# Performance work log

Measured on AMD Instinct MI355X. Metric: run time of the kernel, lower is better.

The kernel has to match this reference:

```python
import jax, jax.numpy as jnp
import numpy as np

CDIM = 32
SCALES = (1, 16, 64, 256, 1024, 4096)  # last entry == T
INV_TEMP = 100.0
ENT_W = 0.1
COMMIT_W = 0.2
Q_SCALE = 1.0 / float(np.sqrt(CDIM))


def _interp_area(x, pt):
    # x: [B, T, C] -> [B, pt, C]; T divisible by pt so 'area' == block mean
    B, T, C = x.shape
    return x.reshape(B, pt, T // pt, C).mean(axis=2)


def _interp_linear(x, T):
    # x: [B, pt, C] -> [B, T, C]; mode='linear', align_corners=False
    pt = x.shape[1]
    pos = (jnp.arange(T, dtype=jnp.float32) + 0.5) * (pt / T) - 0.5
    pos = jnp.clip(pos, 0.0, pt - 1.0)
    lo = jnp.floor(pos).astype(jnp.int32)
    hi = jnp.minimum(lo + 1, pt - 1)
    w = (pos - lo.astype(jnp.float32))[None, :, None]
    return x[:, lo] * (1.0 - w) + x[:, hi] * w


def _bsq(f):
    # L2 normalize (torch F.normalize: clamp_min on norm)
    f = f / jnp.maximum(jnp.linalg.norm(f, axis=-1, keepdims=True), 1e-12)
    # sign quantize with STE
    zhat = jnp.where(f > 0, Q_SCALE, -Q_SCALE).astype(f.dtype)
    quantized = f + jax.lax.stop_gradient(zhat - f)
    # soft entropy loss
    p = jax.nn.sigmoid(-4.0 * f * (INV_TEMP / float(np.sqrt(CDIM))))
    prob = jnp.stack([p, 1.0 - p], axis=-1)  # [B, T, C, 2]
    ent = lambda c: -(c * jnp.log(c + 1e-8)).sum(axis=-1)
    per_sample_entropy = ent(prob).sum(axis=-1).mean()
    avg_prob = prob.mean(axis=(0, 1))  # [C, 2]
    cb_entropy = ent(avg_prob).sum()
    entropy_penalty = (per_sample_entropy - cb_entropy) / INV_TEMP
    commit = ((jax.lax.stop_gradient(quantized) - f) ** 2).sum(axis=-1).mean()
    aux = entropy_penalty * ENT_W + commit * COMMIT_W
    bits = (quantized > 0).astype(jnp.int32)
    return quantized, bits, aux


def setup_inputs() -> dict:
    key = jax.random.key(0)
    B, T, C = 128, SCALES[-1], CDIM
    return {"f_BTC": jax.random.normal(key, (B, T, C), dtype=jnp.float32)}


def reference(f_BTC):
    B, T, C = f_BTC.shape
    quantized_out = jnp.zeros_like(f_BTC)
    residual = f_BTC
    losses, bit_list = [], []
    for pt in SCALES:
        interp_res = _interp_area(residual, pt) if pt != T else residual
        q, bits, loss = _bsq(interp_res)
        q = _interp_linear(q, T) if pt != T else q
        residual = residual - jax.lax.stop_gradient(q)
        quantized_out = quantized_out + q
        bit_list.append(bits)
        losses.append(loss)
    all_losses = jnp.stack(losses, axis=-1)       # [num_scales]
    all_bits = jnp.concatenate(bit_list, axis=1)  # [B, sum(SCALES), C]
    return quantized_out, all_bits, all_losses
```

## Files before the change

### kernel.cpp

```cpp
#include <hip/hip_runtime.h>
#include <hip/hip_bf16.h>
#include <cstddef>
#include <cstdint>

#define NB 128
#define NT 4096
#define NC 32
#define BITROWS 5457
#define QV_ROWS 1361
#define QOUT_ELEMS (NB*NT*NC)
#define BITS_ELEMS (NB*BITROWS*NC)

#define ACC_OFF  22298624
#define S16_OFF  22302720

__device__ __constant__ float kQSC = 0.17677669529663687f;
__device__ __constant__ float kSIG = 17.67766952966369f;

__device__ __forceinline__ float interp_eval(const float* __restrict__ q, int P, int t, int c) {
  float pos = ((float)t + 0.5f) * ((float)P * (1.0f / 4096.0f)) - 0.5f;
  pos = fminf(fmaxf(pos, 0.0f), (float)(P - 1));
  const int lo = (int)pos;
  const int hi = min(lo + 1, P - 1);
  const float w = pos - (float)lo;
  const float a = __fmul_rn(q[lo * NC + c], 1.0f - w);
  const float b = __fmul_rn(q[hi * NC + c], w);
  return __fadd_rn(a, b);
}

__device__ __forceinline__ void process_elem(
    float msum, float invn, int b, int rowOff, int j, int c,
    float* qlsRow, float* __restrict__ qvG, float* __restrict__ bitsG,
    float& entA, float& comA, float& pA)
{
  const float m = msum * invn;
  float ss = m * m;
  #pragma unroll
  for (int mk = 16; mk; mk >>= 1) ss += __shfl_xor(ss, mk, 32);
  const float den = fmaxf(sqrtf(ss), 1e-12f);
  const float fn = m / den;
  const bool bit = fn > 0.0f;
  const float zh = bit ? kQSC : -kQSC;
  const float qvv = fn + (zh - fn);
  if (qlsRow) qlsRow[c] = qvv;
  qvG[(size_t)b * (QV_ROWS * NC) + (size_t)(rowOff + j) * NC + c] = qvv;
  bitsG[(size_t)b * (BITROWS * NC) + (size_t)(rowOff + j) * NC + c] = bit ? 1.0f : 0.0f;
  const float arg = (-4.0f * fn) * kSIG;
  const float p = 1.0f / (1.0f + __expf(-arg));
  const float ent = -(p * __logf(p + 1e-8f) + (1.0f - p) * __logf((1.0f - p) + 1e-8f));
  const float d = qvv - fn;
  entA += ent; comA += d * d; pA += p;
}

__device__ __forceinline__ void reduce_losses(
    int sIdx, float entA, float comA, float pA, int tid, int nWaves,
    double* __restrict__ acc, float* redE, float* redC, float* redP)
{
  float e = entA, cm = comA;
  #pragma unroll
  for (int mk = 32; mk; mk >>= 1) { e += __shfl_xor(e, mk, 64); cm += __shfl_xor(cm, mk, 64); }
  const float p = pA + __shfl_xor(pA, 32, 64);
  const int w = tid >> 6, lane = tid & 63;
  if (lane == 0) { redE[w] = e; redC[w] = cm; }
  if (lane < 32) redP[w * 32 + lane] = p;
  __syncthreads();
  if (tid == 0) {
    double te = 0.0, tc = 0.0;
    for (int i = 0; i < nWaves; ++i) { te += (double)redE[i]; tc += (double)redC[i]; }
    atomicAdd(&acc[sIdx], te);
    atomicAdd(&acc[6 + sIdx], tc);
  }
  if (tid < 32) {
    float tp = 0.0f;
    for (int i = 0; i < nWaves; ++i) tp += redP[i * 32 + tid];
    atomicAdd(&acc[12 + sIdx * 32 + tid], (double)tp);
  }
  __syncthreads();
}

__global__ __launch_bounds__(256) void k_sum16(const float* __restrict__ f, float* __restrict__ S16) {
  const int idx = blockIdx.x * 256 + threadIdx.x;
  if (idx >= NB * 256 * NC) return;
  const int c = idx & 31;
  const int j = (idx >> 5) & 255;
  const int b = idx >> 13;
  const float* p = f + (size_t)b * (NT * NC) + (size_t)j * 16 * NC + c;
  float s = 0.0f;
  #pragma unroll
  for (int k = 0; k < 16; ++k) s += p[k * NC];
  S16[idx] = s;
}

__global__ __launch_bounds__(1024) void k_coarse(
    const float* __restrict__ S16g, float* __restrict__ qv,
    float* __restrict__ bitsOut, double* __restrict__ acc)
{
  __shared__ float S[256 * NC];
  __shared__ float qls[81 * NC];
  __shared__ float red[1024];
  __shared__ float redE[16], redC[16], redP[16 * 32];
  const int b = blockIdx.x, tid = threadIdx.x;
  const int c = tid & 31;

  for (int e = tid; e < 256 * NC; e += 1024) S[e] = S16g[(size_t)b * 8192 + e];
  __syncthreads();

  float entA, comA, pA;

  entA = comA = pA = 0.0f;
  {
    const int g = tid >> 5;
    float part = 0.0f;
    #pragma unroll
    for (int j = 0; j < 8; ++j) part += S[(g * 8 + j) * NC + c];
    red[tid] = part;
  }
  __syncthreads();
  if (tid < 32) {
    float msum = 0.0f;
    for (int g = 0; g < 32; ++g) msum += red[g * 32 + tid];
    process_elem(msum, 1.0f / 4096.0f, b, 0, 0, tid, &qls[0], qv, bitsOut, entA, comA, pA);
  }
  reduce_losses(0, entA, comA, pA, tid, 16, acc, redE, redC, redP);
  {
    const float corr = 16.0f * qls[c];
    for (int e = tid; e < 8192; e += 1024) S[e] -= corr;
  }
  __syncthreads();

  entA = comA = pA = 0.0f;
  if (tid < 512) {
    const int j = tid >> 5;
    float msum = 0.0f;
    for (int jj = 0; jj < 16; ++jj) msum += S[(j * 16 + jj) * NC + c];
    process_elem(msum, 1.0f / 256.0f, b, 1, j, c, &qls[(1 + j) * NC], qv, bitsOut, entA, comA, pA);
  }
  reduce_losses(1, entA, comA, pA, tid, 16, acc, redE, redC, redP);
  for (int e = tid; e < 8192; e += 1024) {
    const int jj = e >> 5;
    float cs = 0.0f;
    #pragma unroll
    for (int k = 0; k < 16; ++k) cs += interp_eval(&qls[1 * NC], 16, jj * 16 + k, c);
    S[e] -= cs;
  }
  __syncthreads();

  entA = comA = pA = 0.0f;
  for (int out = tid; out < 2048; out += 1024) {
    const int j = out >> 5;
    float msum = 0.0f;
    #pragma unroll
    for (int jj = 0; jj < 4; ++jj) msum += S[(j * 4 + jj) * NC + c];
    process_elem(msum, 1.0f / 64.0f, b, 17, j, c, &qls[(17 + j) * NC], qv, bitsOut, entA, comA, pA);
  }
  reduce_losses(2, entA, comA, pA, tid, 16, acc, redE, redC, redP);
  for (int e = tid; e < 8192; e += 1024) {
    const int jj = e >> 5;
    float cs = 0.0f;
    #pragma unroll
    for (int k = 0; k < 16; ++k) cs += interp_eval(&qls[17 * NC], 64, jj * 16 + k, c);
    S[e] -= cs;
  }
  __syncthreads();

  entA = comA = pA = 0.0f;
  for (int out = tid; out < 8192; out += 1024) {
    const int j = out >> 5;
    process_elem(S[out], 1.0f / 16.0f, b, 81, j, c, nullptr, qv, bitsOut, entA, comA, pA);
  }
  reduce_losses(3, entA, comA, pA, tid, 16, acc, redE, redC, redP);
}

__global__ __launch_bounds__(256) void k_scale4(
    const float* __restrict__ f, float* __restrict__ qv,
    float* __restrict__ bitsOut, double* __restrict__ acc)
{
  __shared__ float ql[337 * NC];
  __shared__ float redE[16], redC[16], redP[16 * 32];
  const int b = blockIdx.x >> 4, seg = blockIdx.x & 15;
  const int tid = threadIdx.x, c = tid & 31, rloc = tid >> 5;
  for (int e = tid; e < 337 * NC; e += 256) ql[e] = qv[(size_t)b * (QV_ROWS * NC) + e];
  __syncthreads();
  float entA = 0.0f, comA = 0.0f, pA = 0.0f;
  for (int pass = 0; pass < 8; ++pass) {
    const int i = seg * 64 + pass * 8 + rloc;
    const float* fp = f + (size_t)b * (NT * NC) + (size_t)i * 4 * NC + c;
    float msum = 0.0f;
    #pragma unroll
    for (int k = 0; k < 4; ++k) {
      const int t = i * 4 + k;
      float r = fp[k * NC];
      r -= interp_eval(&ql[0],        1,   t, c);
      r -= interp_eval(&ql[1 * NC],   16,  t, c);
      r -= interp_eval(&ql[17 * NC],  64,  t, c);
      r -= interp_eval(&ql[81 * NC],  256, t, c);
      msum += r;
    }
    process_elem(msum, 0.25f, b, 337, i, c, nullptr, qv, bitsOut, entA, comA, pA);
  }
  reduce_losses(4, entA, comA, pA, tid, 4, acc, redE, redC, redP);
}

__global__ __launch_bounds__(256) void k_final(
    const float* __restrict__ f, const float* __restrict__ qv,
    float* __restrict__ qout, float* __restrict__ bitsOut, double* __restrict__ acc)
{
  __shared__ float ql[337 * NC];
  __shared__ float ql4[66 * NC];
  __shared__ float redE[16], redC[16], redP[16 * 32];
  const int b = blockIdx.x >> 4, seg = blockIdx.x & 15;
  const int tid = threadIdx.x, c = tid & 31, rloc = tid >> 5;
  const int t0 = seg * 256;
  for (int e = tid; e < 337 * NC; e += 256) ql[e] = qv[(size_t)b * (QV_ROWS * NC) + e];
  const int lo0 = max(0, t0 / 4 - 1);
  const int lo1 = min(1023, t0 / 4 + 64);
  const int n4 = (lo1 - lo0 + 1) * NC;
  for (int e = tid; e < n4; e += 256)
    ql4[e] = qv[(size_t)b * (QV_ROWS * NC) + (size_t)(337 + lo0) * NC + e];
  __syncthreads();
  float entA = 0.0f, comA = 0.0f, pA = 0.0f;
  for (int pass = 0; pass < 32; ++pass) {
    const int t = t0 + pass * 8 + rloc;
    const float fv = f[(size_t)b * (NT * NC) + (size_t)t * NC + c];
    const float q0 = interp_eval(&ql[0],       1,   t, c);
    const float q1 = interp_eval(&ql[1 * NC],  16,  t, c);
    const float q2 = interp_eval(&ql[17 * NC], 64,  t, c);
    const float q3 = interp_eval(&ql[81 * NC], 256, t, c);
    float pos = ((float)t + 0.5f) * 0.25f - 0.5f;
    pos = fminf(fmaxf(pos, 0.0f), 1023.0f);
    const int lo = (int)pos;
    const int hi = min(lo + 1, 1023);
    const float w = pos - (float)lo;
    const float q4 = __fadd_rn(__fmul_rn(ql4[(lo - lo0) * NC + c], 1.0f - w),
                               __fmul_rn(ql4[(hi - lo0) * NC + c], w));
    float r = fv;
    r -= q0; r -= q1; r -= q2; r -= q3; r -= q4;
    float qs = q0; qs += q1; qs += q2; qs += q3; qs += q4;
    float ss = r * r;
    #pragma unroll
    for (int mk = 16; mk; mk >>= 1) ss += __shfl_xor(ss, mk, 32);
    const float den = fmaxf(sqrtf(ss), 1e-12f);
    const float fn = r / den;
    const bool bit = fn > 0.0f;
    const float zh = bit ? kQSC : -kQSC;
    const float qvv = fn + (zh - fn);
    qout[(size_t)b * (NT * NC) + (size_t)t * NC + c] = qs + qvv;
    bitsOut[(size_t)b * (BITROWS * NC) + (size_t)(1361 + t) * NC + c] = bit ? 1.0f : 0.0f;
    const float arg = (-4.0f * fn) * kSIG;
    const float p = 1.0f / (1.0f + __expf(-arg));
    entA += -(p * __logf(p + 1e-8f) + (1.0f - p) * __logf((1.0f - p) + 1e-8f));
    const float d = qvv - fn;
    comA += d * d;
    pA += p;
  }
  reduce_losses(5, entA, comA, pA, tid, 4, acc, redE, redC, redP);
}

__global__ void k_losses(const double* __restrict__ acc, float* __restrict__ out) {
  const int s = threadIdx.x;
  if (s >= 6) return;
  const int pts[6] = {1, 16, 64, 256, 1024, 4096};
  const double n = 128.0 * (double)pts[s];
  const double pse = acc[s] / n;
  const double commit = acc[6 + s] / n;
  double cbe = 0.0;
  for (int c = 0; c < 32; ++c) {
    const double ap = acc[12 + s * 32 + c] / n;
    cbe += -(ap * log(ap + 1e-8) + (1.0 - ap) * log((1.0 - ap) + 1e-8));
  }
  const double pen = (pse - cbe) / 100.0;
  out[s] = (float)(pen * 0.1 + commit * 0.2);
}

extern "C" void kernel_launch(void* const* d_in, const int* in_sizes, int n_in,
                              void* d_out, int out_size, void* d_ws, size_t ws_size,
                              hipStream_t stream) {
  const float* f = (const float*)d_in[0];
  float* qout = (float*)d_out;
  float* bitsOut = qout + QOUT_ELEMS;
  float* lossesOut = qout + (QOUT_ELEMS + BITS_ELEMS);
  float* qv = (float*)d_ws;
  double* acc = (double*)((char*)d_ws + ACC_OFF);
  float* S16 = (float*)((char*)d_ws + S16_OFF);

  hipMemsetAsync(acc, 0, 204 * sizeof(double), stream);
  k_sum16<<<4096, 256, 0, stream>>>(f, S16);
  k_coarse<<<NB, 1024, 0, stream>>>(S16, qv, bitsOut, acc);
  k_scale4<<<NB * 16, 256, 0, stream>>>(f, qv, bitsOut, acc);
  k_final<<<NB * 16, 256, 0, stream>>>(f, qv, qout, bitsOut, acc);
  k_losses<<<1, 64, 0, stream>>>(acc, lossesOut);
}
```

Measured before the change: 378.3 us.

## Fuse scale-1024 and final scale into one kernel with halo recompute

Merges the separate scale-4 (1024-row) and final (4096) kernels into one fused kernel. Each block covers 128 timesteps plus a small halo, computes the residual once into shared memory, and quantizes the 1024-scale rows locally instead of round-tripping them through global workspace. Only coarse-scale rows are kept in the workspace, and k_sum16 is vectorized with float4 loads. This removes a second full read of f and a kernel launch, at the cost of redundant halo computation and more shared memory per block.

```diff
diff --git a/kernel.cpp b/kernel.cpp
--- a/kernel.cpp
+++ b/kernel.cpp
@@ -7,12 +7,12 @@
 #define NT 4096
 #define NC 32
 #define BITROWS 5457
-#define QV_ROWS 1361
+#define CQ_ROWS 337
 #define QOUT_ELEMS (NB*NT*NC)
 #define BITS_ELEMS (NB*BITROWS*NC)
 
-#define ACC_OFF  22298624
-#define S16_OFF  22302720
+#define ACC_OFF  5521408
+#define S16_OFF  5523456
 
 __device__ __constant__ float kQSC = 0.17677669529663687f;
 __device__ __constant__ float kSIG = 17.67766952966369f;
@@ -28,28 +28,51 @@
   return __fadd_rn(a, b);
 }
 
+__device__ __forceinline__ float interp_evalS(const float* __restrict__ qbase, int sb, int P,
+                                              float scale, int t, int c) {
+  float pos = ((float)t + 0.5f) * scale - 0.5f;
+  pos = fminf(fmaxf(pos, 0.0f), (float)(P - 1));
+  const int lo = (int)pos;
+  const int hi = min(lo + 1, P - 1);
+  const float w = pos - (float)lo;
+  const float a = __fmul_rn(qbase[(lo - sb) * NC + c], 1.0f - w);
+  const float b = __fmul_rn(qbase[(hi - sb) * NC + c], w);
+  return __fadd_rn(a, b);
+}
+
+__device__ __forceinline__ void quant_core(float m, float& qvv, float& fn, bool& bit) {
+  float ss = m * m;
+  #pragma unroll
+  for (int mk = 16; mk; mk >>= 1) ss += __shfl_xor(ss, mk, 32);
+  const float den = fmaxf(sqrtf(ss), 1e-12f);
+  fn = m / den;
+  bit = fn > 0.0f;
+  const float zh = bit ? kQSC : -kQSC;
+  qvv = fn + (zh - fn);
+}
+
+__device__ __forceinline__ void loss_piece(float fn, float qvv, float& p, float& ent, float& c2) {
+  const float arg = (-4.0f * fn) * kSIG;
+  p = __builtin_amdgcn_rcpf(1.0f + __expf(-arg));
+  ent = -(p * __logf(p + 1e-8f) + (1.0f - p) * __logf((1.0f - p) + 1e-8f));
+  const float d = qvv - fn;
+  c2 = d * d;
+}
+
 __device__ __forceinline__ void process_elem(
     float msum, float invn, int b, int rowOff, int j, int c,
     float* qlsRow, float* __restrict__ qvG, float* __restrict__ bitsG,
     float& entA, float& comA, float& pA)
 {
   const float m = msum * invn;
-  float ss = m * m;
-  #pragma unroll
-  for (int mk = 16; mk; mk >>= 1) ss += __shfl_xor(ss, mk, 32);
-  const float den = fmaxf(sqrtf(ss), 1e-12f);
-  const float fn = m / den;
-  const bool bit = fn > 0.0f;
-  const float zh = bit ? kQSC : -kQSC;
-  const float qvv = fn + (zh - fn);
+  float qvv, fn; bool bit;
+  quant_core(m, qvv, fn, bit);
   if (qlsRow) qlsRow[c] = qvv;
-  qvG[(size_t)b * (QV_ROWS * NC) + (size_t)(rowOff + j) * NC + c] = qvv;
+  qvG[(size_t)b * (CQ_ROWS * NC) + (size_t)(rowOff + j) * NC + c] = qvv;
   bitsG[(size_t)b * (BITROWS * NC) + (size_t)(rowOff + j) * NC + c] = bit ? 1.0f : 0.0f;
-  const float arg = (-4.0f * fn) * kSIG;
-  const float p = 1.0f / (1.0f + __expf(-arg));
-  const float ent = -(p * __logf(p + 1e-8f) + (1.0f - p) * __logf((1.0f - p) + 1e-8f));
-  const float d = qvv - fn;
-  entA += ent; comA += d * d; pA += p;
+  float p, ent, c2;
+  loss_piece(fn, qvv, p, ent, c2);
+  entA += ent; comA += c2; pA += p;
 }
 
 __device__ __forceinline__ void reduce_losses(
@@ -78,17 +101,19 @@
   __syncthreads();
 }
 
-__global__ __launch_bounds__(256) void k_sum16(const float* __restrict__ f, float* __restrict__ S16) {
+__global__ __launch_bounds__(256) void k_sum16(const float4* __restrict__ f4, float4* __restrict__ S4) {
   const int idx = blockIdx.x * 256 + threadIdx.x;
-  if (idx >= NB * 256 * NC) return;
-  const int c = idx & 31;
-  const int j = (idx >> 5) & 255;
-  const int b = idx >> 13;
-  const float* p = f + (size_t)b * (NT * NC) + (size_t)j * 16 * NC + c;
-  float s = 0.0f;
+  const int c4 = idx & 7;
+  const int j  = (idx >> 3) & 255;
+  const int b  = idx >> 11;
+  const float4* p = f4 + (size_t)b * 32768 + (size_t)j * 128 + c4;
+  float4 s = {0.f, 0.f, 0.f, 0.f};
   #pragma unroll
-  for (int k = 0; k < 16; ++k) s += p[k * NC];
-  S16[idx] = s;
+  for (int k = 0; k < 16; ++k) {
+    const float4 v = p[k * 8];
+    s.x += v.x; s.y += v.y; s.z += v.z; s.w += v.w;
+  }
+  S4[idx] = s;
 }
 
 __global__ __launch_bounds__(1024) void k_coarse(
@@ -171,87 +196,83 @@
   reduce_losses(3, entA, comA, pA, tid, 16, acc, redE, redC, redP);
 }
 
-__global__ __launch_bounds__(256) void k_scale4(
-    const float* __restrict__ f, float* __restrict__ qv,
-    float* __restrict__ bitsOut, double* __restrict__ acc)
-{
-  __shared__ float ql[337 * NC];
-  __shared__ float redE[16], redC[16], redP[16 * 32];
-  const int b = blockIdx.x >> 4, seg = blockIdx.x & 15;
-  const int tid = threadIdx.x, c = tid & 31, rloc = tid >> 5;
-  for (int e = tid; e < 337 * NC; e += 256) ql[e] = qv[(size_t)b * (QV_ROWS * NC) + e];
-  __syncthreads();
-  float entA = 0.0f, comA = 0.0f, pA = 0.0f;
-  for (int pass = 0; pass < 8; ++pass) {
-    const int i = seg * 64 + pass * 8 + rloc;
-    const float* fp = f + (size_t)b * (NT * NC) + (size_t)i * 4 * NC + c;
-    float msum = 0.0f;
-    #pragma unroll
-    for (int k = 0; k < 4; ++k) {
-      const int t = i * 4 + k;
-      float r = fp[k * NC];
-      r -= interp_eval(&ql[0],        1,   t, c);
-      r -= interp_eval(&ql[1 * NC],   16,  t, c);
-      r -= interp_eval(&ql[17 * NC],  64,  t, c);
-      r -= interp_eval(&ql[81 * NC],  256, t, c);
-      msum += r;
-    }
-    process_elem(msum, 0.25f, b, 337, i, c, nullptr, qv, bitsOut, entA, comA, pA);
-  }
-  reduce_losses(4, entA, comA, pA, tid, 4, acc, redE, redC, redP);
-}
-
-__global__ __launch_bounds__(256) void k_final(
+__global__ __launch_bounds__(256) void k_fused(
     const float* __restrict__ f, const float* __restrict__ qv,
     float* __restrict__ qout, float* __restrict__ bitsOut, double* __restrict__ acc)
 {
-  __shared__ float ql[337 * NC];
-  __shared__ float ql4[66 * NC];
-  __shared__ float redE[16], redC[16], redP[16 * 32];
-  const int b = blockIdx.x >> 4, seg = blockIdx.x & 15;
+  __shared__ float qsl[33 * NC];
+  __shared__ float rp[136 * NC];
+  __shared__ float qpre[128 * NC];
+  __shared__ float q4r[34 * NC];
+  __shared__ float redE[4], redC[4], redP[4 * 32];
+
+  const int b = blockIdx.x >> 5, seg = blockIdx.x & 31;
+  const int t0 = seg << 7;
   const int tid = threadIdx.x, c = tid & 31, rloc = tid >> 5;
-  const int t0 = seg * 256;
-  for (int e = tid; e < 337 * NC; e += 256) ql[e] = qv[(size_t)b * (QV_ROWS * NC) + e];
-  const int lo0 = max(0, t0 / 4 - 1);
-  const int lo1 = min(1023, t0 / 4 + 64);
-  const int n4 = (lo1 - lo0 + 1) * NC;
-  for (int e = tid; e < n4; e += 256)
-    ql4[e] = qv[(size_t)b * (QV_ROWS * NC) + (size_t)(337 + lo0) * NC + e];
-  __syncthreads();
-  float entA = 0.0f, comA = 0.0f, pA = 0.0f;
-  for (int pass = 0; pass < 32; ++pass) {
+  const int R0 = max(t0 / 4 - 1, 0);
+  const int R1 = min(t0 / 4 + 32, 1023);
+  const int tb = R0 * 4, tn = (R1 - R0 + 1) * 4;
+  const int S2B = min(max(t0 / 64 - 1, 0), 60);
+  const int S3B = min(max(tb / 16 - 1, 0), 244);
+  const size_t fb = (size_t)b * (NT * NC);
+  const size_t bbits = (size_t)b * (BITROWS * NC);
+
+  for (int e = tid; e < 33 * NC; e += 256) {
+    const int r = e >> 5, cc = e & 31;
+    int grow;
+    if (e < 544)        grow = r;
+    else if (e < 672)   grow = 17 + S2B + (r - 17);
+    else                grow = 81 + S3B + (r - 21);
+    qsl[e] = qv[(size_t)b * (CQ_ROWS * NC) + (size_t)grow * NC + cc];
+  }
+  __syncthreads();
+
+  for (int pass = 0; pass < 17; ++pass) {
+    const int tt = tb + pass * 8 + rloc;
+    if (tt < tb + tn) {
+      const float fv = f[fb + (size_t)tt * NC + c];
+      float r = fv - qsl[c];
+      r -= interp_evalS(qsl + 32,  0,   16,  0.00390625f, tt, c);
+      r -= interp_evalS(qsl + 544, S2B, 64,  0.015625f,   tt, c);
+      r -= interp_evalS(qsl + 672, S3B, 256, 0.0625f,     tt, c);
+      rp[(tt - tb) * NC + c] = r;
+      if (tt >= t0 && tt < t0 + 128) qpre[(tt - t0) * NC + c] = fv - r;
+    }
+  }
+  __syncthreads();
+
+  float entA = 0.f, comA = 0.f, pA = 0.f;
+  for (int pass = 0; pass < 5; ++pass) {
+    const int j = R0 + pass * 8 + rloc;
+    if (j <= R1) {
+      const int base = (4 * j - tb) * NC + c;
+      const float msum = rp[base] + rp[base + NC] + rp[base + 2 * NC] + rp[base + 3 * NC];
+      float qvv, fn; bool bit;
+      quant_core(msum * 0.25f, qvv, fn, bit);
+      q4r[(j - R0) * NC + c] = qvv;
+      if (j >= t0 / 4 && j < t0 / 4 + 32) {
+        bitsOut[bbits + (size_t)(337 + j) * NC + c] = bit ? 1.0f : 0.0f;
+        float p, ent, c2;
+        loss_piece(fn, qvv, p, ent, c2);
+        entA += ent; comA += c2; pA += p;
+      }
+    }
+  }
+  reduce_losses(4, entA, comA, pA, tid, 4, acc, redE, redC, redP);
+
+  entA = comA = pA = 0.f;
+  for (int pass = 0; pass < 16; ++pass) {
     const int t = t0 + pass * 8 + rloc;
-    const float fv = f[(size_t)b * (NT * NC) + (size_t)t * NC + c];
-    const float q0 = interp_eval(&ql[0],       1,   t, c);
-    const float q1 = interp_eval(&ql[1 * NC],  16,  t, c);
-    const float q2 = interp_eval(&ql[17 * NC], 64,  t, c);
-    const float q3 = interp_eval(&ql[81 * NC], 256, t, c);
-    float pos = ((float)t + 0.5f) * 0.25f - 0.5f;
-    pos = fminf(fmaxf(pos, 0.0f), 1023.0f);
-    const int lo = (int)pos;
-    const int hi = min(lo + 1, 1023);
-    const float w = pos - (float)lo;
-    const float q4 = __fadd_rn(__fmul_rn(ql4[(lo - lo0) * NC + c], 1.0f - w),
-                               __fmul_rn(ql4[(hi - lo0) * NC + c], w));
-    float r = fv;
-    r -= q0; r -= q1; r -= q2; r -= q3; r -= q4;
-    float qs = q0; qs += q1; qs += q2; qs += q3; qs += q4;
-    float ss = r * r;
-    #pragma unroll
-    for (int mk = 16; mk; mk >>= 1) ss += __shfl_xor(ss, mk, 32);
-    const float den = fmaxf(sqrtf(ss), 1e-12f);
-    const float fn = r / den;
-    const bool bit = fn > 0.0f;
-    const float zh = bit ? kQSC : -kQSC;
-    const float qvv = fn + (zh - fn);
-    qout[(size_t)b * (NT * NC) + (size_t)t * NC + c] = qs + qvv;
-    bitsOut[(size_t)b * (BITROWS * NC) + (size_t)(1361 + t) * NC + c] = bit ? 1.0f : 0.0f;
-    const float arg = (-4.0f * fn) * kSIG;
-    const float p = 1.0f / (1.0f + __expf(-arg));
-    entA += -(p * __logf(p + 1e-8f) + (1.0f - p) * __logf((1.0f - p) + 1e-8f));
-    const float d = qvv - fn;
-    comA += d * d;
-    pA += p;
+    const float rpv = rp[(t - tb) * NC + c];
+    const float q4 = interp_evalS(q4r, R0, 1024, 0.25f, t, c);
+    const float r = rpv - q4;
+    float qvv, fn; bool bit;
+    quant_core(r, qvv, fn, bit);
+    qout[fb + (size_t)t * NC + c] = (qpre[(t - t0) * NC + c] + q4) + qvv;
+    bitsOut[bbits + (size_t)(1361 + t) * NC + c] = bit ? 1.0f : 0.0f;
+    float p, ent, c2;
+    loss_piece(fn, qvv, p, ent, c2);
+    entA += ent; comA += c2; pA += p;
   }
   reduce_losses(5, entA, comA, pA, tid, 4, acc, redE, redC, redP);
 }
@@ -284,9 +305,8 @@
   float* S16 = (float*)((char*)d_ws + S16_OFF);
 
   hipMemsetAsync(acc, 0, 204 * sizeof(double), stream);
-  k_sum16<<<4096, 256, 0, stream>>>(f, S16);
+  k_sum16<<<1024, 256, 0, stream>>>((const float4*)f, (float4*)S16);
   k_coarse<<<NB, 1024, 0, stream>>>(S16, qv, bitsOut, acc);
-  k_scale4<<<NB * 16, 256, 0, stream>>>(f, qv, bitsOut, acc);
-  k_final<<<NB * 16, 256, 0, stream>>>(f, qv, qout, bitsOut, acc);
+  k_fused<<<NB * 32, 256, 0, stream>>>(f, qv, qout, bitsOut, acc);
   k_losses<<<1, 64, 0, stream>>>(acc, lossesOut);
 }
```

After: 384.1 us. Within noise of the previous version (+1.5%).
